# Kernel optimization log

Measured on AMD Instinct MI355X. Metric: run time of the kernel, lower is better.

Reference implementation:

```python
import jax, jax.numpy as jnp
import numpy as np

NBINS = 9
CELL = 16
H, W = 256, 128          # win_size=(128,256) is (width,height)
CY, CX = H // CELL, W // CELL
BY, BX = CY - 1, CX - 1
FEAT = BY * BX * 4 * NBINS      # 3780
PAD_TO = 4096


def _hog(imgs):
    # imgs: [B, H, W, 3] float32 in [0,255]
    B = imgs.shape[0]
    x = jnp.pad(imgs, ((0, 0), (1, 1), (1, 1), (0, 0)), mode='edge')
    dx = x[:, 1:-1, 2:, :] - x[:, 1:-1, :-2, :]   # [-1,0,1] horizontal
    dy = x[:, 2:, 1:-1, :] - x[:, :-2, 1:-1, :]   # [-1,0,1] vertical
    # per-pixel: pick the channel with the largest gradient magnitude (cv2 HOG)
    mag2 = dx * dx + dy * dy
    ch = jnp.argmax(mag2, axis=-1, keepdims=True)
    dx = jnp.take_along_axis(dx, ch, axis=-1)[..., 0]
    dy = jnp.take_along_axis(dy, ch, axis=-1)[..., 0]
    mag = jnp.sqrt(dx * dx + dy * dy)
    ang = jnp.mod(jnp.arctan2(dy, dx), jnp.pi)    # unsigned gradients [0,pi)
    # bilinear orientation binning (cv2: hidx = angle*nbins/pi - 0.5)
    pos = ang * (NBINS / jnp.pi) - 0.5
    b0 = jnp.floor(pos)
    frac = pos - b0
    b0i = jnp.mod(b0.astype(jnp.int32), NBINS)
    b1i = jnp.mod(b0i + 1, NBINS)
    w0 = mag * (1.0 - frac)
    w1 = mag * frac
    # per-cell orientation histograms: [B, CY, CX, NBINS]
    hists = []
    for k in range(NBINS):
        vk = jnp.where(b0i == k, w0, 0.0) + jnp.where(b1i == k, w1, 0.0)
        vk = vk.reshape(B, CY, CELL, CX, CELL).sum(axis=(2, 4))
        hists.append(vk)
    cell_hist = jnp.stack(hists, axis=-1)
    # overlapping 2x2-cell blocks, stride = 1 cell -> [B, BY, BX, 4, NBINS]
    blk = jnp.stack([
        cell_hist[:, :-1, :-1], cell_hist[:, :-1, 1:],
        cell_hist[:, 1:, :-1], cell_hist[:, 1:, 1:]], axis=3)
    v = blk.reshape(B, BY, BX, 4 * NBINS)
    # L2-Hys block normalization (cv2: scale=1/(||v||+sz*0.1), clip 0.2, renorm)
    sz = float(4 * NBINS)
    n1 = jnp.sqrt(jnp.sum(v * v, axis=-1, keepdims=True))
    v = v / (n1 + sz * 0.1)
    v = jnp.minimum(v, 0.2)
    n2 = jnp.sqrt(jnp.sum(v * v, axis=-1, keepdims=True))
    v = v / (n2 + 1e-3)
    feat = v.reshape(B, FEAT)
    return jnp.pad(feat, ((0, 0), (0, PAD_TO - FEAT)))


def setup_inputs() -> dict:
    key = jax.random.key(0)
    k1, k2, k3 = jax.random.split(key, 3)
    B = 512
    images = jax.random.uniform(k1, (B, 3, H, W), dtype=jnp.float32) * 255.0
    targets = jax.random.randint(k2, (B,), 0, 751, dtype=jnp.int64 if jax.config.jax_enable_x64 else jnp.int32).astype(jnp.int32)
    camid = jax.random.randint(k3, (B,), 0, 8, dtype=jnp.int32)
    return {"images": images, "targets": targets, "camid": camid}


def reference(images, targets, camid):
    imgs = jnp.transpose(images, (0, 2, 3, 1))  # NCHW -> NHWC
    feat = _hog(imgs)                           # [B, 4096]
    return feat, targets, camid
```

## Files before the change

kernel.cpp:

```cpp
#include <hip/hip_runtime.h>

#define HOG_PI  3.14159265358979323846f
#define HOG_PI2 1.57079632679489661923f

typedef float f2 __attribute__((ext_vector_type(2)));

__device__ __forceinline__ float dpp_from_left(float x) {
  return __int_as_float(__builtin_amdgcn_mov_dpp(__float_as_int(x), 0x130, 0xF, 0xF, true));
}
__device__ __forceinline__ float dpp_from_right(float x) {
  return __int_as_float(__builtin_amdgcn_mov_dpp(__float_as_int(x), 0x138, 0xF, 0xF, true));
}

__device__ __forceinline__ void px_tail(
    float dxs, float dys, float g, float base, float* __restrict__ row) {
  const float mag = __builtin_amdgcn_sqrtf(g);
  const bool oct = fabsf(dys) > fabsf(dxs);
  float th = oct ? (HOG_PI2 - base) : base;
  if (dxs * dys < 0.0f) th = HOG_PI - th;
  const float pos = th * (9.0f / HOG_PI) - 0.5f;
  const float bf = floorf(pos);
  const float frac = pos - bf;
  const int b0 = (int)bf;
  const int b0i = (b0 < 0) ? 8 : b0;
  const float w0 = mag * (1.0f - frac);
  const float w1 = mag * frac;
  float* p = row + b0i;
  const float a0 = p[0];
  const float a1 = p[1];
  p[0] = a0 + w0;
  p[1] = a1 + w1;
}

__device__ __forceinline__ void accum_quad(
    const float4 c0, const float4 c1, const float4 c2,
    const float4 p0, const float4 p1, const float4 p2,
    const float4 n0, const float4 n1, const float4 n2,
    int xq, float* __restrict__ partT) {
  f2 dx[3][2], dy[3][2], g[3][2];
#pragma unroll
  for (int c = 0; c < 3; ++c) {
    const float4 cc = (c == 0) ? c0 : (c == 1) ? c1 : c2;
    const float4 pp = (c == 0) ? p0 : (c == 1) ? p1 : p2;
    const float4 nn = (c == 0) ? n0 : (c == 1) ? n1 : n2;
    float lf = dpp_from_left(cc.w);
    float rf = dpp_from_right(cc.x);
    if (xq == 0) lf = cc.x;
    if (xq == 31) rf = cc.w;
    dx[c][0] = (f2){cc.y, cc.z} - (f2){lf, cc.x};
    dx[c][1] = (f2){cc.w, rf} - (f2){cc.y, cc.z};
    dy[c][0] = (f2){nn.x, nn.y} - (f2){pp.x, pp.y};
    dy[c][1] = (f2){nn.z, nn.w} - (f2){pp.z, pp.w};
    g[c][0] = dx[c][0] * dx[c][0] + dy[c][0] * dy[c][0];
    g[c][1] = dx[c][1] * dx[c][1] + dy[c][1] * dy[c][1];
  }
#pragma unroll
  for (int p = 0; p < 2; ++p) {
    float dxsA = dx[0][p].x, dysA = dy[0][p].x, gA = g[0][p].x;
    if (g[1][p].x > gA) { dxsA = dx[1][p].x; dysA = dy[1][p].x; gA = g[1][p].x; }
    if (g[2][p].x > gA) { dxsA = dx[2][p].x; dysA = dy[2][p].x; gA = g[2][p].x; }
    float dxsB = dx[0][p].y, dysB = dy[0][p].y, gB = g[0][p].y;
    if (g[1][p].y > gB) { dxsB = dx[1][p].y; dysB = dy[1][p].y; gB = g[1][p].y; }
    if (g[2][p].y > gB) { dxsB = dx[2][p].y; dysB = dy[2][p].y; gB = g[2][p].y; }
    const float mnA = fminf(fabsf(dxsA), fabsf(dysA));
    const float mxA = fmaxf(fmaxf(fabsf(dxsA), fabsf(dysA)), 1e-30f);
    const float aA = mnA * __builtin_amdgcn_rcpf(mxA);
    const float mnB = fminf(fabsf(dxsB), fabsf(dysB));
    const float mxB = fmaxf(fmaxf(fabsf(dxsB), fabsf(dysB)), 1e-30f);
    const float aB = mnB * __builtin_amdgcn_rcpf(mxB);
    const f2 av = {aA, aB};
    const f2 sq = av * av;
    const f2 base =
        ((((f2)(0.0208351f) * sq - (f2)(0.0851330f)) * sq + (f2)(0.1801410f)) *
             sq - (f2)(0.3302995f)) * sq * av + (f2)(0.9998660f) * av;
    px_tail(dxsA, dysA, gA, base.x, partT + ((2 * p) & 1) * 10);
    px_tail(dxsB, dysB, gB, base.y, partT + ((2 * p + 1) & 1) * 10);
  }
}

__global__ __launch_bounds__(512, 2) void hog_kernel(
    const float* __restrict__ img, const int* __restrict__ targets,
    const int* __restrict__ camid, float* __restrict__ out, int B) {
  const int b = blockIdx.x;
  const int t = threadIdx.x;
  const float* im = img + (size_t)b * (3 * 256 * 128);

  __shared__ float lds[512 * 20];
  float* const partT = lds + t * 20;

  const int xq = t & 31;
  const int m = t >> 5;
  const int x0 = xq * 4;
  const int cx = xq >> 2;
  const int r0 = m * 16;

#pragma unroll
  for (int j = 0; j < 20; ++j) partT[j] = 0.0f;

  const float* ch0 = im;
  const float* ch1 = im + 32768;
  const float* ch2 = im + 65536;

  const int rp = (r0 == 0) ? 0 : r0 - 1;
  float4 p0 = *(const float4*)(ch0 + rp * 128 + x0);
  float4 p1 = *(const float4*)(ch1 + rp * 128 + x0);
  float4 p2 = *(const float4*)(ch2 + rp * 128 + x0);
  float4 c0 = *(const float4*)(ch0 + r0 * 128 + x0);
  float4 c1 = *(const float4*)(ch1 + r0 * 128 + x0);
  float4 c2 = *(const float4*)(ch2 + r0 * 128 + x0);
  float4 n0 = *(const float4*)(ch0 + (r0 + 1) * 128 + x0);
  float4 n1 = *(const float4*)(ch1 + (r0 + 1) * 128 + x0);
  float4 n2 = *(const float4*)(ch2 + (r0 + 1) * 128 + x0);

#pragma unroll 1
  for (int r = 0; r < 16; ++r) {
    const int y2 = r0 + r + 2;
    const int yc = (y2 > 255) ? 255 : y2;
    const float4 f0 = *(const float4*)(ch0 + yc * 128 + x0);
    const float4 f1 = *(const float4*)(ch1 + yc * 128 + x0);
    const float4 f2v = *(const float4*)(ch2 + yc * 128 + x0);

    accum_quad(c0, c1, c2, p0, p1, p2, n0, n1, n2, xq, partT);

    p0 = c0; p1 = c1; p2 = c2;
    c0 = n0; c1 = n1; c2 = n2;
    n0 = f0; n1 = f1; n2 = f2v;
  }

  float hv[9];
#pragma unroll
  for (int k = 0; k < 9; ++k) hv[k] = partT[k] + partT[10 + k];
  hv[0] += partT[9] + partT[19];
  __syncthreads();

  float (*cellh)[8][9] = (float (*)[8][9])lds;
#pragma unroll
  for (int k = 0; k < 9; ++k) {
    float v = hv[k];
    v += __shfl_xor(v, 1, 64);
    v += __shfl_xor(v, 2, 64);
    if ((xq & 3) == 0) cellh[m][cx][k] = v;
  }
  __syncthreads();

  float* outF = out + (size_t)b * 4096;
  if (t < 105) {
    const int by = t / 7;
    const int bx = t - by * 7;
    float v[36];
#pragma unroll
    for (int q = 0; q < 4; ++q) {
      const int cy = by + (q >> 1);
      const int ccx = bx + (q & 1);
#pragma unroll
      for (int k = 0; k < 9; ++k) v[q * 9 + k] = cellh[cy][ccx][k];
    }
    float ss = 0.0f;
#pragma unroll
    for (int jj = 0; jj < 36; ++jj) ss += v[jj] * v[jj];
    const float s1 = 1.0f / (sqrtf(ss) + 3.6f);
    float ss2 = 0.0f;
#pragma unroll
    for (int jj = 0; jj < 36; ++jj) {
      v[jj] = fminf(v[jj] * s1, 0.2f);
      ss2 += v[jj] * v[jj];
    }
    const float s2 = 1.0f / (sqrtf(ss2) + 1e-3f);
    float4* dst = (float4*)(outF + (by * 7 + bx) * 36);
#pragma unroll
    for (int q = 0; q < 9; ++q)
      dst[q] = make_float4(v[4 * q] * s2, v[4 * q + 1] * s2,
                           v[4 * q + 2] * s2, v[4 * q + 3] * s2);
  }
  for (int i = 3780 + t; i < 4096; i += 512) outF[i] = 0.0f;
  if (t == 400) out[(size_t)B * 4096 + b] = (float)targets[b];
  if (t == 401) out[(size_t)B * 4096 + B + b] = (float)camid[b];
}

extern "C" void kernel_launch(void* const* d_in, const int* in_sizes, int n_in,
                              void* d_out, int out_size, void* d_ws, size_t ws_size,
                              hipStream_t stream) {
  const float* images = (const float*)d_in[0];
  const int* targets = (const int*)d_in[1];
  const int* camid = (const int*)d_in[2];
  float* out = (float*)d_out;
  const int B = in_sizes[1];
  hipLaunchKernelGGL(hog_kernel, dim3(B), dim3(512), 0, stream,
                     images, targets, camid, out, B);
}
```

Measured before the change: 43.53 us.

## Use 1024-thread blocks with 8-row strips and cross-wave cell reduction

Doubles threads per image so each thread handles 8 rows instead of 16. The two half-strips of a 16-row cell are merged with an extra xor-32 shuffle inside each wave. The gradient computation is restructured per pixel pair to lower register pressure, and the launch bounds now ask for 8 waves per EU. This is meant to raise memory-level parallelism and occupancy, at the cost of double the LDS per block and a one-row halo re-read for each strip.

```diff
diff --git a/kernel.cpp b/kernel.cpp
--- a/kernel.cpp
+++ b/kernel.cpp
@@ -37,31 +37,33 @@
     const float4 p0, const float4 p1, const float4 p2,
     const float4 n0, const float4 n1, const float4 n2,
     int xq, float* __restrict__ partT) {
-  f2 dx[3][2], dy[3][2], g[3][2];
-#pragma unroll
-  for (int c = 0; c < 3; ++c) {
-    const float4 cc = (c == 0) ? c0 : (c == 1) ? c1 : c2;
-    const float4 pp = (c == 0) ? p0 : (c == 1) ? p1 : p2;
-    const float4 nn = (c == 0) ? n0 : (c == 1) ? n1 : n2;
-    float lf = dpp_from_left(cc.w);
-    float rf = dpp_from_right(cc.x);
-    if (xq == 0) lf = cc.x;
-    if (xq == 31) rf = cc.w;
-    dx[c][0] = (f2){cc.y, cc.z} - (f2){lf, cc.x};
-    dx[c][1] = (f2){cc.w, rf} - (f2){cc.y, cc.z};
-    dy[c][0] = (f2){nn.x, nn.y} - (f2){pp.x, pp.y};
-    dy[c][1] = (f2){nn.z, nn.w} - (f2){pp.z, pp.w};
-    g[c][0] = dx[c][0] * dx[c][0] + dy[c][0] * dy[c][0];
-    g[c][1] = dx[c][1] * dx[c][1] + dy[c][1] * dy[c][1];
-  }
 #pragma unroll
   for (int p = 0; p < 2; ++p) {
-    float dxsA = dx[0][p].x, dysA = dy[0][p].x, gA = g[0][p].x;
-    if (g[1][p].x > gA) { dxsA = dx[1][p].x; dysA = dy[1][p].x; gA = g[1][p].x; }
-    if (g[2][p].x > gA) { dxsA = dx[2][p].x; dysA = dy[2][p].x; gA = g[2][p].x; }
-    float dxsB = dx[0][p].y, dysB = dy[0][p].y, gB = g[0][p].y;
-    if (g[1][p].y > gB) { dxsB = dx[1][p].y; dysB = dy[1][p].y; gB = g[1][p].y; }
-    if (g[2][p].y > gB) { dxsB = dx[2][p].y; dysB = dy[2][p].y; gB = g[2][p].y; }
+    f2 dx[3], dy[3], g[3];
+#pragma unroll
+    for (int c = 0; c < 3; ++c) {
+      const float4 cc = (c == 0) ? c0 : (c == 1) ? c1 : c2;
+      const float4 pp = (c == 0) ? p0 : (c == 1) ? p1 : p2;
+      const float4 nn = (c == 0) ? n0 : (c == 1) ? n1 : n2;
+      if (p == 0) {
+        float lf = dpp_from_left(cc.w);
+        if (xq == 0) lf = cc.x;
+        dx[c] = (f2){cc.y, cc.z} - (f2){lf, cc.x};
+        dy[c] = (f2){nn.x, nn.y} - (f2){pp.x, pp.y};
+      } else {
+        float rf = dpp_from_right(cc.x);
+        if (xq == 31) rf = cc.w;
+        dx[c] = (f2){cc.w, rf} - (f2){cc.y, cc.z};
+        dy[c] = (f2){nn.z, nn.w} - (f2){pp.z, pp.w};
+      }
+      g[c] = dx[c] * dx[c] + dy[c] * dy[c];
+    }
+    float dxsA = dx[0].x, dysA = dy[0].x, gA = g[0].x;
+    if (g[1].x > gA) { dxsA = dx[1].x; dysA = dy[1].x; gA = g[1].x; }
+    if (g[2].x > gA) { dxsA = dx[2].x; dysA = dy[2].x; gA = g[2].x; }
+    float dxsB = dx[0].y, dysB = dy[0].y, gB = g[0].y;
+    if (g[1].y > gB) { dxsB = dx[1].y; dysB = dy[1].y; gB = g[1].y; }
+    if (g[2].y > gB) { dxsB = dx[2].y; dysB = dy[2].y; gB = g[2].y; }
     const float mnA = fminf(fabsf(dxsA), fabsf(dysA));
     const float mxA = fmaxf(fmaxf(fabsf(dxsA), fabsf(dysA)), 1e-30f);
     const float aA = mnA * __builtin_amdgcn_rcpf(mxA);
@@ -73,26 +75,26 @@
     const f2 base =
         ((((f2)(0.0208351f) * sq - (f2)(0.0851330f)) * sq + (f2)(0.1801410f)) *
              sq - (f2)(0.3302995f)) * sq * av + (f2)(0.9998660f) * av;
-    px_tail(dxsA, dysA, gA, base.x, partT + ((2 * p) & 1) * 10);
-    px_tail(dxsB, dysB, gB, base.y, partT + ((2 * p + 1) & 1) * 10);
+    px_tail(dxsA, dysA, gA, base.x, partT);
+    px_tail(dxsB, dysB, gB, base.y, partT + 10);
   }
 }
 
-__global__ __launch_bounds__(512, 2) void hog_kernel(
+__global__ __launch_bounds__(1024, 8) void hog_kernel(
     const float* __restrict__ img, const int* __restrict__ targets,
     const int* __restrict__ camid, float* __restrict__ out, int B) {
   const int b = blockIdx.x;
   const int t = threadIdx.x;
   const float* im = img + (size_t)b * (3 * 256 * 128);
 
-  __shared__ float lds[512 * 20];
+  __shared__ float lds[1024 * 20];
   float* const partT = lds + t * 20;
 
   const int xq = t & 31;
-  const int m = t >> 5;
+  const int s = t >> 5;
   const int x0 = xq * 4;
   const int cx = xq >> 2;
-  const int r0 = m * 16;
+  const int r0 = s * 8;
 
 #pragma unroll
   for (int j = 0; j < 20; ++j) partT[j] = 0.0f;
@@ -108,23 +110,19 @@
   float4 c0 = *(const float4*)(ch0 + r0 * 128 + x0);
   float4 c1 = *(const float4*)(ch1 + r0 * 128 + x0);
   float4 c2 = *(const float4*)(ch2 + r0 * 128 + x0);
-  float4 n0 = *(const float4*)(ch0 + (r0 + 1) * 128 + x0);
-  float4 n1 = *(const float4*)(ch1 + (r0 + 1) * 128 + x0);
-  float4 n2 = *(const float4*)(ch2 + (r0 + 1) * 128 + x0);
 
 #pragma unroll 1
-  for (int r = 0; r < 16; ++r) {
-    const int y2 = r0 + r + 2;
-    const int yc = (y2 > 255) ? 255 : y2;
-    const float4 f0 = *(const float4*)(ch0 + yc * 128 + x0);
-    const float4 f1 = *(const float4*)(ch1 + yc * 128 + x0);
-    const float4 f2v = *(const float4*)(ch2 + yc * 128 + x0);
+  for (int r = 0; r < 8; ++r) {
+    const int y = r0 + r;
+    const int yn = (y == 255) ? 255 : y + 1;
+    const float4 n0 = *(const float4*)(ch0 + yn * 128 + x0);
+    const float4 n1 = *(const float4*)(ch1 + yn * 128 + x0);
+    const float4 n2 = *(const float4*)(ch2 + yn * 128 + x0);
 
     accum_quad(c0, c1, c2, p0, p1, p2, n0, n1, n2, xq, partT);
 
     p0 = c0; p1 = c1; p2 = c2;
     c0 = n0; c1 = n1; c2 = n2;
-    n0 = f0; n1 = f1; n2 = f2v;
   }
 
   float hv[9];
@@ -134,12 +132,14 @@
   __syncthreads();
 
   float (*cellh)[8][9] = (float (*)[8][9])lds;
+  const int lane = t & 63;
 #pragma unroll
   for (int k = 0; k < 9; ++k) {
     float v = hv[k];
     v += __shfl_xor(v, 1, 64);
     v += __shfl_xor(v, 2, 64);
-    if ((xq & 3) == 0) cellh[m][cx][k] = v;
+    v += __shfl_xor(v, 32, 64);
+    if ((xq & 3) == 0 && lane < 32) cellh[t >> 6][cx][k] = v;
   }
   __syncthreads();
 
@@ -172,7 +172,7 @@
       dst[q] = make_float4(v[4 * q] * s2, v[4 * q + 1] * s2,
                            v[4 * q + 2] * s2, v[4 * q + 3] * s2);
   }
-  for (int i = 3780 + t; i < 4096; i += 512) outF[i] = 0.0f;
+  for (int i = 3780 + t; i < 4096; i += 1024) outF[i] = 0.0f;
   if (t == 400) out[(size_t)B * 4096 + b] = (float)targets[b];
   if (t == 401) out[(size_t)B * 4096 + B + b] = (float)camid[b];
 }
@@ -185,6 +185,6 @@
   const int* camid = (const int*)d_in[2];
   float* out = (float*)d_out;
   const int B = in_sizes[1];
-  hipLaunchKernelGGL(hog_kernel, dim3(B), dim3(512), 0, stream,
+  hipLaunchKernelGGL(hog_kernel, dim3(B), dim3(1024), 0, stream,
                      images, targets, camid, out, B);
 }
```

New measurement: 54.01 us. 1.24x slower.
